# Kernel tuning notes

Hardware: AMD Instinct MI355X
Metric: run time of the kernel (lower is better)

The kernel has to match this reference:

```python
import math
import jax, jax.numpy as jnp
import numpy as np

THETA = 2.0 ** 16
TWO_PI = 2.0 * math.pi


def _freqs(N):
    # quantize(arange(N), 2) = floor(t/2)*2 -> paired frequencies
    idx = jnp.floor(jnp.arange(N, dtype=jnp.float32) / 2.0) * 2.0
    return 1.0 / (THETA ** (idx / N)) / TWO_PI  # (N,)


def _rope(v, cos, sin):
    # rotate pairs: (-v_odd, v_even) interleaved back to original layout
    v_rot = jnp.stack((-v[..., 1::2], v[..., ::2]), axis=-1).reshape(v.shape)
    return v * cos + v_rot * sin


def setup_inputs() -> dict:
    key = jax.random.key(0)
    k1, k2 = jax.random.split(key)
    B, nh, T, N, D = 1, 4, 2048, 8192, 256
    Q = jax.random.normal(k1, (B, nh, T, N), dtype=jnp.float32) * 0.02
    V = jax.random.normal(k2, (B, 1, T, D), dtype=jnp.float32)
    return {"Q": Q, "V": V}


def reference(Q, V):
    # Q: (B, nh, T, N) sparse neuron space; V: (B, 1, T, D) embedding space; K is Q
    T, N = Q.shape[2], Q.shape[3]
    freqs = _freqs(N)
    phases = jnp.arange(T, dtype=jnp.float32)[:, None] * freqs[None, :]  # (T, N)
    ang = (phases % 1.0) * TWO_PI
    cos, sin = jnp.cos(ang), jnp.sin(ang)
    QR = _rope(Q, cos, sin)  # (B, nh, T, N)
    scores = jnp.einsum('bhtn,bhsn->bhts', QR, QR)  # (B, nh, T, T)
    causal = jnp.tril(jnp.ones((T, T), dtype=bool), k=-1)  # strictly lower
    scores = jnp.where(causal, scores, 0.0)
    # V broadcasts over heads: (B, nh, T, T) @ (B, 1, T, D) -> (B, nh, T, D)
    return jnp.matmul(scores, V)
```

## Files before the change

### kernel.cpp

```cpp
#include <hip/hip_runtime.h>

#define LDS_AS __attribute__((address_space(3)))
#define GLB_AS __attribute__((address_space(1)))

typedef __attribute__((ext_vector_type(8))) short bf16x8;
typedef __attribute__((ext_vector_type(4))) float f32x4;

static constexpr int NH = 4;
static constexpr int T  = 2048;
static constexpr int N  = 8192;
static constexpr int D  = 256;

__device__ inline unsigned short f2bf(float f) {
    unsigned int u = __float_as_uint(f);
    u += 0x7FFFu + ((u >> 16) & 1u);
    return (unsigned short)(u >> 16);
}

__device__ inline void gl2lds16(const void* g, void* l) {
    __builtin_amdgcn_global_load_lds((GLB_AS void*)g, (LDS_AS void*)l, 16, 0, 0);
}

__global__ void rope_kernel(const float* __restrict__ Q, unsigned short* __restrict__ QR) {
    int g = blockIdx.x * 256 + threadIdx.x;
    int base = g << 2;
    int n = base & (N - 1);
    int t = (base >> 13) & (T - 1);
    const float4 q = *(const float4*)(Q + (size_t)base);
    float tf = (float)t;
    const float inv2pi = 0.15915494309189535f;
    float f0 = exp2f((float)n       * (-1.0f / 512.0f)) * inv2pi;
    float f1 = exp2f((float)(n + 2) * (-1.0f / 512.0f)) * inv2pi;
    float r0 = tf * f0; r0 -= floorf(r0);
    float r1 = tf * f1; r1 -= floorf(r1);
    float s0 = __builtin_amdgcn_sinf(r0), c0 = __builtin_amdgcn_cosf(r0);
    float s1 = __builtin_amdgcn_sinf(r1), c1 = __builtin_amdgcn_cosf(r1);
    ushort4 o;
    o.x = f2bf(q.x * c0 - q.y * s0);
    o.y = f2bf(q.y * c0 + q.x * s0);
    o.z = f2bf(q.z * c1 - q.w * s1);
    o.w = f2bf(q.w * c1 + q.z * s1);
    *(ushort4*)(QR + (size_t)base) = o;
}

__global__ void vt_kernel(const float* __restrict__ V, unsigned short* __restrict__ Vt) {
    __shared__ unsigned short tile[64 * 65];
    int tb = blockIdx.x >> 2, db = blockIdx.x & 3;
    int t0 = tb * 64, d0 = db * 64;
    int tid = threadIdx.x;
    #pragma unroll
    for (int r = 0; r < 16; r++) {
        int idx = tid + r * 256;
        int tl = idx >> 6, dl = idx & 63;
        tile[tl * 65 + dl] = f2bf(V[(size_t)(t0 + tl) * D + d0 + dl]);
    }
    __syncthreads();
    #pragma unroll
    for (int r = 0; r < 16; r++) {
        int idx = tid + r * 256;
        int dl = idx >> 6, tl = idx & 63;
        Vt[(size_t)(d0 + dl) * T + t0 + tl] = tile[tl * 65 + dl];
    }
}

__global__ __launch_bounds__(256, 2) void gemm1_kernel(const unsigned short* __restrict__ QR,
                                                       unsigned short* __restrict__ S, int KS) {
    __shared__ __align__(16) unsigned short As[3][128 * 32];
    __shared__ __align__(16) unsigned short Bs[3][256 * 32];

    int bx = blockIdx.x;
    int per_h = 72 * KS;
    int h = bx / per_h;
    int rem = bx % per_h;
    int task = rem / KS;
    int ks = rem % KS;
    int bi = 0, cum = 0;
    for (; bi < 16; bi++) { int nb = (bi >> 1) + 1; if (cum + nb > task) break; cum += nb; }
    int bj = task - cum;

    const unsigned short* A = QR + (size_t)h * T * N + (size_t)bi * 128 * N;
    const unsigned short* B = QR + (size_t)h * T * N + (size_t)bj * 256 * N;

    int KN = N / KS;
    int k_begin = ks * KN;
    int nit = KN / 32;

    int tid = threadIdx.x;
    int lane = tid & 63, wave = tid >> 6;
    int wm = wave >> 1, wn = wave & 1;
    int quad = lane >> 4, l16 = lane & 15;
    int srow = tid >> 2;
    int scol = (tid & 3) * 8;

    f32x4 acc[4][8];
    #pragma unroll
    for (int i = 0; i < 4; i++)
        #pragma unroll
        for (int j = 0; j < 8; j++)
            #pragma unroll
            for (int r = 0; r < 4; r++) acc[i][j][r] = 0.0f;

    #pragma unroll
    for (int p = 0; p < 2; p++) {
        int k0 = k_begin + p * 32;
        gl2lds16(A + (size_t)srow * N + k0 + scol,         &As[p][srow * 32 + scol]);
        gl2lds16(A + (size_t)(srow + 64) * N + k0 + scol,  &As[p][(srow + 64) * 32 + scol]);
        gl2lds16(B + (size_t)srow * N + k0 + scol,         &Bs[p][srow * 32 + scol]);
        gl2lds16(B + (size_t)(srow + 64) * N + k0 + scol,  &Bs[p][(srow + 64) * 32 + scol]);
        gl2lds16(B + (size_t)(srow + 128) * N + k0 + scol, &Bs[p][(srow + 128) * 32 + scol]);
        gl2lds16(B + (size_t)(srow + 192) * N + k0 + scol, &Bs[p][(srow + 192) * 32 + scol]);
    }

    int cur = 0, nxt2 = 2;
    for (int it = 0; it < nit; it++) {
        if (it + 1 < nit) {
            asm volatile("s_waitcnt vmcnt(6)" ::: "memory");
        } else {
            asm volatile("s_waitcnt vmcnt(0)" ::: "memory");
        }
        __builtin_amdgcn_s_barrier();
        __builtin_amdgcn_sched_barrier(0);

        bf16x8 a[4], b[8];
        #pragma unroll
        for (int i = 0; i < 4; i++)
            a[i] = *(const bf16x8*)&As[cur][(wm * 64 + i * 16 + l16) * 32 + quad * 8];
        #pragma unroll
        for (int j = 0; j < 8; j++)
            b[j] = *(const bf16x8*)&Bs[cur][(wn * 128 + j * 16 + l16) * 32 + quad * 8];

        if (it + 2 < nit) {
            int k0 = k_begin + (it + 2) * 32;
            gl2lds16(A + (size_t)srow * N + k0 + scol,         &As[nxt2][srow * 32 + scol]);
            gl2lds16(A + (size_t)(srow + 64) * N + k0 + scol,  &As[nxt2][(srow + 64) * 32 + scol]);
            gl2lds16(B + (size_t)srow * N + k0 + scol,         &Bs[nxt2][srow * 32 + scol]);
            gl2lds16(B + (size_t)(srow + 64) * N + k0 + scol,  &Bs[nxt2][(srow + 64) * 32 + scol]);
            gl2lds16(B + (size_t)(srow + 128) * N + k0 + scol, &Bs[nxt2][(srow + 128) * 32 + scol]);
            gl2lds16(B + (size_t)(srow + 192) * N + k0 + scol, &Bs[nxt2][(srow + 192) * 32 + scol]);
        }

        __builtin_amdgcn_s_setprio(1);
        #pragma unroll
        for (int j = 0; j < 8; j++)
            #pragma unroll
            for (int i = 0; i < 4; i++)
                acc[i][j] = __builtin_amdgcn_mfma_f32_16x16x32_bf16(a[i], b[j], acc[i][j], 0, 0, 0);
        __builtin_amdgcn_s_setprio(0);

        cur  = (cur  == 2) ? 0 : cur  + 1;
        nxt2 = (nxt2 == 2) ? 0 : nxt2 + 1;
    }

    unsigned short* Sh = S + (size_t)ks * NH * T * T + (size_t)h * T * T;
    #pragma unroll
    for (int i = 0; i < 4; i++) {
        int t_base = bi * 128 + wm * 64 + i * 16 + quad * 4;
        #pragma unroll
        for (int j = 0; j < 8; j++) {
            int s_g = bj * 256 + wn * 128 + j * 16 + l16;
            #pragma unroll
            for (int r = 0; r < 4; r++) {
                int t_g = t_base + r;
                float v = (s_g < t_g) ? acc[i][j][r] : 0.0f;
                Sh[(size_t)t_g * T + s_g] = f2bf(v);
            }
        }
    }
}

__global__ __launch_bounds__(256) void gemm2_kernel(const unsigned short* __restrict__ S,
                                                    const unsigned short* __restrict__ Vt,
                                                    float* __restrict__ out, int KS) {
    __shared__ __align__(16) unsigned short As[2][128 * 32];
    __shared__ __align__(16) unsigned short Bs[2][128 * 32];

    int bx = blockIdx.x;
    int per_h = 2 * 72;
    int h = bx / per_h;
    int rem = bx % per_h;
    int dblk = rem / 72;
    int tc = rem % 72;
    int bi = 0, cum = 0;
    for (; bi < 16; bi++) { int nc = (bi + 2) >> 1; if (cum + nc > tc) break; cum += nc; }
    int c = tc - cum;

    int kend = (bi + 1) * 128;
    int cstart = c * 256;
    int clen = min(256, kend - cstart);
    int cpk = clen >> 5;
    int ls = (KS == 4) ? 2 : (KS == 2) ? 1 : 0;
    int nit = cpk << ls;

    const unsigned short* Sh = S + (size_t)h * T * T + (size_t)bi * 128 * T + cstart;
    const size_t sstride = (size_t)NH * T * T;
    const unsigned short* B = Vt + (size_t)dblk * 128 * T + cstart;

    int tid = threadIdx.x;
    int lane = tid & 63, wave = tid >> 6;
    int wm = wave >> 1, wn = wave & 1;
    int quad = lane >> 4, l16 = lane & 15;
    int srow = tid >> 2;
    int scol = (tid & 3) * 8;

    f32x4 acc[4][4];
    #pragma unroll
    for (int i = 0; i < 4; i++)
        #pragma unroll
        for (int j = 0; j < 4; j++)
            #pragma unroll
            for (int r = 0; r < 4; r++) acc[i][j][r] = 0.0f;

    gl2lds16(Sh + (size_t)srow * T + scol,        &As[0][srow * 32 + scol]);
    gl2lds16(Sh + (size_t)(srow + 64) * T + scol, &As[0][(srow + 64) * 32 + scol]);
    gl2lds16(B + (size_t)srow * T + scol,         &Bs[0][srow * 32 + scol]);
    gl2lds16(B + (size_t)(srow + 64) * T + scol,  &Bs[0][(srow + 64) * 32 + scol]);

    bf16x8 b[4];
    for (int i = 0; i < nit; i++) {
        int k0i = i >> ls;
        int ks  = i & (KS - 1);
        __syncthreads();
        if (i + 1 < nit) {
            int ksn = (i + 1) & (KS - 1);
            int k0n = (i + 1) >> ls;
            const unsigned short* An = Sh + (size_t)ksn * sstride + k0n * 32;
            int pan = (i + 1) & 1;
            gl2lds16(An + (size_t)srow * T + scol,        &As[pan][srow * 32 + scol]);
            gl2lds16(An + (size_t)(srow + 64) * T + scol, &As[pan][(srow + 64) * 32 + scol]);
            if (ksn == 0) {
                const unsigned short* Bn = B + k0n * 32;
                int pbn = k0n & 1;
                gl2lds16(Bn + (size_t)srow * T + scol,        &Bs[pbn][srow * 32 + scol]);
                gl2lds16(Bn + (size_t)(srow + 64) * T + scol, &Bs[pbn][(srow + 64) * 32 + scol]);
            }
        }

        int pa = i & 1, pb = k0i & 1;
        if (ks == 0) {
            #pragma unroll
            for (int j = 0; j < 4; j++)
                b[j] = *(const bf16x8*)&Bs[pb][(wn * 64 + j * 16 + l16) * 32 + quad * 8];
        }
        bf16x8 a[4];
        #pragma unroll
        for (int ii = 0; ii < 4; ii++)
            a[ii] = *(const bf16x8*)&As[pa][(wm * 64 + ii * 16 + l16) * 32 + quad * 8];
        #pragma unroll
        for (int ii = 0; ii < 4; ii++)
            #pragma unroll
            for (int j = 0; j < 4; j++)
                acc[ii][j] = __builtin_amdgcn_mfma_f32_16x16x32_bf16(a[ii], b[j], acc[ii][j], 0, 0, 0);
    }

    float* oh = out + (size_t)h * T * D;
    #pragma unroll
    for (int i = 0; i < 4; i++) {
        int t_base = bi * 128 + wm * 64 + i * 16 + quad * 4;
        #pragma unroll
        for (int j = 0; j < 4; j++) {
            int d_g = dblk * 128 + wn * 64 + j * 16 + l16;
            #pragma unroll
            for (int r = 0; r < 4; r++) {
                int t_g = t_base + r;
                atomicAdd(&oh[(size_t)t_g * D + d_g], acc[i][j][r]);
            }
        }
    }
}

extern "C" void kernel_launch(void* const* d_in, const int* in_sizes, int n_in,
                              void* d_out, int out_size, void* d_ws, size_t ws_size,
                              hipStream_t stream) {
    const float* Q = (const float*)d_in[0];
    const float* V = (const float*)d_in[1];
    float* out = (float*)d_out;

    const size_t qr_elems = (size_t)NH * T * N;
    const size_t vt_elems = (size_t)D * T;
    const size_t s_elems  = (size_t)NH * T * T;

    int KS = 1;
    for (int cand : {4, 2, 1}) {
        if (ws_size >= (qr_elems + vt_elems + (size_t)cand * s_elems) * sizeof(unsigned short)) {
            KS = cand; break;
        }
    }
    if (ws_size < (qr_elems + vt_elems + (size_t)KS * s_elems) * sizeof(unsigned short)) return;

    unsigned short* QR = (unsigned short*)d_ws;
    unsigned short* Vt = QR + qr_elems;
    unsigned short* S  = Vt + vt_elems;

    rope_kernel<<<(NH * T * N / 4) / 256, 256, 0, stream>>>(Q, QR);
    vt_kernel<<<(T / 64) * (D / 64), 256, 0, stream>>>(V, Vt);
    gemm1_kernel<<<NH * 72 * KS, 256, 0, stream>>>(QR, S, KS);
    hipMemsetAsync(d_out, 0, (size_t)out_size * sizeof(float), stream);
    gemm2_kernel<<<NH * 2 * 40 * 0 + NH * 2 * 72, 256, 0, stream>>>(S, Vt, out, KS);
}
```

Measured before the change: 578.6 us.

## Switch QK^T GEMM to 32x32x16 MFMA with fragment-ordered LDS layout

Replaces the 16x16x32 bf16 MFMA tiles in the score GEMM with 32x32x16 MFMA, so each wave holds 2x4 accumulators of 16 floats instead of 4x8 of 4. Global-to-LDS loads now write a fragment-contiguous layout, so each lane reads its operand as one linear 16-byte chunk at lane*8, which removes strided row reads and likely LDS bank conflicts. The aim is fewer MFMA issues and LDS reads per k-step. The epilogue is remapped to the 32x32 output register layout, and its scattered bf16 stores may be less coalesced.

```diff
diff --git a/kernel.cpp b/kernel.cpp
--- a/kernel.cpp
+++ b/kernel.cpp
@@ -5,6 +5,7 @@
 
 typedef __attribute__((ext_vector_type(8))) short bf16x8;
 typedef __attribute__((ext_vector_type(4))) float f32x4;
+typedef __attribute__((ext_vector_type(16))) float f32x16;
 
 static constexpr int NH = 4;
 static constexpr int T  = 2048;
@@ -65,15 +66,15 @@
 
 __global__ __launch_bounds__(256, 2) void gemm1_kernel(const unsigned short* __restrict__ QR,
                                                        unsigned short* __restrict__ S, int KS) {
-    __shared__ __align__(16) unsigned short As[3][128 * 32];
-    __shared__ __align__(16) unsigned short Bs[3][256 * 32];
+    __shared__ __align__(16) unsigned short As[3][4096];
+    __shared__ __align__(16) unsigned short Bs[3][8192];
 
     int bx = blockIdx.x;
     int per_h = 72 * KS;
     int h = bx / per_h;
     int rem = bx % per_h;
     int task = rem / KS;
-    int ks = rem % KS;
+    int ksp = rem % KS;
     int bi = 0, cum = 0;
     for (; bi < 16; bi++) { int nb = (bi >> 1) + 1; if (cum + nb > task) break; cum += nb; }
     int bj = task - cum;
@@ -82,33 +83,36 @@
     const unsigned short* B = QR + (size_t)h * T * N + (size_t)bj * 256 * N;
 
     int KN = N / KS;
-    int k_begin = ks * KN;
+    int k_begin = ksp * KN;
     int nit = KN / 32;
 
     int tid = threadIdx.x;
     int lane = tid & 63, wave = tid >> 6;
     int wm = wave >> 1, wn = wave & 1;
-    int quad = lane >> 4, l16 = lane & 15;
-    int srow = tid >> 2;
-    int scol = (tid & 3) * 8;
-
-    f32x4 acc[4][8];
-    #pragma unroll
-    for (int i = 0; i < 4; i++)
-        #pragma unroll
-        for (int j = 0; j < 8; j++)
-            #pragma unroll
-            for (int r = 0; r < 4; r++) acc[i][j][r] = 0.0f;
+
+    int blk0 = wave;
+    int rowA = ((blk0 >> 1) << 5) + (lane & 31);
+    int kkA  = ((blk0 & 1) << 4) + ((lane >> 5) << 3);
+    const unsigned short* Asrc = A + (size_t)rowA * N + kkA;
+    const unsigned short* Bsrc = B + (size_t)rowA * N + kkA;
+
+    f32x16 acc[2][4];
+    #pragma unroll
+    for (int i = 0; i < 2; i++)
+        #pragma unroll
+        for (int j = 0; j < 4; j++)
+            #pragma unroll
+            for (int r = 0; r < 16; r++) acc[i][j][r] = 0.0f;
 
     #pragma unroll
     for (int p = 0; p < 2; p++) {
         int k0 = k_begin + p * 32;
-        gl2lds16(A + (size_t)srow * N + k0 + scol,         &As[p][srow * 32 + scol]);
-        gl2lds16(A + (size_t)(srow + 64) * N + k0 + scol,  &As[p][(srow + 64) * 32 + scol]);
-        gl2lds16(B + (size_t)srow * N + k0 + scol,         &Bs[p][srow * 32 + scol]);
-        gl2lds16(B + (size_t)(srow + 64) * N + k0 + scol,  &Bs[p][(srow + 64) * 32 + scol]);
-        gl2lds16(B + (size_t)(srow + 128) * N + k0 + scol, &Bs[p][(srow + 128) * 32 + scol]);
-        gl2lds16(B + (size_t)(srow + 192) * N + k0 + scol, &Bs[p][(srow + 192) * 32 + scol]);
+        gl2lds16(Asrc + k0,                   &As[p][tid * 8]);
+        gl2lds16(Asrc + (size_t)64 * N + k0,  &As[p][2048 + tid * 8]);
+        gl2lds16(Bsrc + k0,                   &Bs[p][tid * 8]);
+        gl2lds16(Bsrc + (size_t)64 * N + k0,  &Bs[p][2048 + tid * 8]);
+        gl2lds16(Bsrc + (size_t)128 * N + k0, &Bs[p][4096 + tid * 8]);
+        gl2lds16(Bsrc + (size_t)192 * N + k0, &Bs[p][6144 + tid * 8]);
     }
 
     int cur = 0, nxt2 = 2;
@@ -121,47 +125,55 @@
         __builtin_amdgcn_s_barrier();
         __builtin_amdgcn_sched_barrier(0);
 
-        bf16x8 a[4], b[8];
-        #pragma unroll
-        for (int i = 0; i < 4; i++)
-            a[i] = *(const bf16x8*)&As[cur][(wm * 64 + i * 16 + l16) * 32 + quad * 8];
-        #pragma unroll
-        for (int j = 0; j < 8; j++)
-            b[j] = *(const bf16x8*)&Bs[cur][(wn * 128 + j * 16 + l16) * 32 + quad * 8];
+        bf16x8 a2[2][2], b2[4][2];
+        #pragma unroll
+        for (int i = 0; i < 2; i++)
+            #pragma unroll
+            for (int kk = 0; kk < 2; kk++)
+                a2[i][kk] = *(const bf16x8*)&As[cur][(((wm * 2 + i) * 2 + kk) << 9) + lane * 8];
+        #pragma unroll
+        for (int j = 0; j < 4; j++)
+            #pragma unroll
+            for (int kk = 0; kk < 2; kk++)
+                b2[j][kk] = *(const bf16x8*)&Bs[cur][(((wn * 4 + j) * 2 + kk) << 9) + lane * 8];
 
         if (it + 2 < nit) {
             int k0 = k_begin + (it + 2) * 32;
-            gl2lds16(A + (size_t)srow * N + k0 + scol,         &As[nxt2][srow * 32 + scol]);
-            gl2lds16(A + (size_t)(srow + 64) * N + k0 + scol,  &As[nxt2][(srow + 64) * 32 + scol]);
-            gl2lds16(B + (size_t)srow * N + k0 + scol,         &Bs[nxt2][srow * 32 + scol]);
-            gl2lds16(B + (size_t)(srow + 64) * N + k0 + scol,  &Bs[nxt2][(srow + 64) * 32 + scol]);
-            gl2lds16(B + (size_t)(srow + 128) * N + k0 + scol, &Bs[nxt2][(srow + 128) * 32 + scol]);
-            gl2lds16(B + (size_t)(srow + 192) * N + k0 + scol, &Bs[nxt2][(srow + 192) * 32 + scol]);
+            gl2lds16(Asrc + k0,                   &As[nxt2][tid * 8]);
+            gl2lds16(Asrc + (size_t)64 * N + k0,  &As[nxt2][2048 + tid * 8]);
+            gl2lds16(Bsrc + k0,                   &Bs[nxt2][tid * 8]);
+            gl2lds16(Bsrc + (size_t)64 * N + k0,  &Bs[nxt2][2048 + tid * 8]);
+            gl2lds16(Bsrc + (size_t)128 * N + k0, &Bs[nxt2][4096 + tid * 8]);
+            gl2lds16(Bsrc + (size_t)192 * N + k0, &Bs[nxt2][6144 + tid * 8]);
         }
 
         __builtin_amdgcn_s_setprio(1);
         #pragma unroll
-        for (int j = 0; j < 8; j++)
-            #pragma unroll
-            for (int i = 0; i < 4; i++)
-                acc[i][j] = __builtin_amdgcn_mfma_f32_16x16x32_bf16(a[i], b[j], acc[i][j], 0, 0, 0);
+        for (int kk = 0; kk < 2; kk++)
+            #pragma unroll
+            for (int j = 0; j < 4; j++)
+                #pragma unroll
+                for (int i = 0; i < 2; i++)
+                    acc[i][j] = __builtin_amdgcn_mfma_f32_32x32x16_bf16(a2[i][kk], b2[j][kk],
+                                                                        acc[i][j], 0, 0, 0);
         __builtin_amdgcn_s_setprio(0);
 
         cur  = (cur  == 2) ? 0 : cur  + 1;
         nxt2 = (nxt2 == 2) ? 0 : nxt2 + 1;
     }
 
-    unsigned short* Sh = S + (size_t)ks * NH * T * T + (size_t)h * T * T;
-    #pragma unroll
-    for (int i = 0; i < 4; i++) {
-        int t_base = bi * 128 + wm * 64 + i * 16 + quad * 4;
-        #pragma unroll
-        for (int j = 0; j < 8; j++) {
-            int s_g = bj * 256 + wn * 128 + j * 16 + l16;
-            #pragma unroll
-            for (int r = 0; r < 4; r++) {
-                int t_g = t_base + r;
-                float v = (s_g < t_g) ? acc[i][j][r] : 0.0f;
+    unsigned short* Sh = S + (size_t)ksp * NH * T * T + (size_t)h * T * T;
+    int col = lane & 31;
+    int rbase = (lane >> 5) * 4;
+    #pragma unroll
+    for (int i = 0; i < 2; i++) {
+        #pragma unroll
+        for (int j = 0; j < 4; j++) {
+            int s_g = bj * 256 + wn * 128 + j * 32 + col;
+            #pragma unroll
+            for (int reg = 0; reg < 16; reg++) {
+                int t_g = bi * 128 + wm * 64 + i * 32 + (reg & 3) + 8 * (reg >> 2) + rbase;
+                float v = (s_g < t_g) ? acc[i][j][reg] : 0.0f;
                 Sh[(size_t)t_g * T + s_g] = f2bf(v);
             }
         }
@@ -295,5 +307,5 @@
     vt_kernel<<<(T / 64) * (D / 64), 256, 0, stream>>>(V, Vt);
     gemm1_kernel<<<NH * 72 * KS, 256, 0, stream>>>(QR, S, KS);
     hipMemsetAsync(d_out, 0, (size_t)out_size * sizeof(float), stream);
-    gemm2_kernel<<<NH * 2 * 40 * 0 + NH * 2 * 72, 256, 0, stream>>>(S, Vt, out, KS);
-}
+    gemm2_kernel<<<NH * 2 * 72, 256, 0, stream>>>(S, Vt, out, KS);
+}
```

Result: slower. 658.9 us (+13.9%).
